# Optimization experiments

Hardware: AMD Instinct MI355X
Metric: run time of the kernel (lower is better)

Reference implementation:

```python
import jax, jax.numpy as jnp
import numpy as np

TEMP = 0.5  # init kwarg `tmp`
NUM_CLASSES = 100


def setup_inputs() -> dict:
    key = jax.random.key(0)
    k1, k2 = jax.random.split(key)
    embedding = jax.random.normal(k1, (8192, 256), dtype=jnp.float32)
    label = jax.random.randint(k2, (8192,), 0, NUM_CLASSES, dtype=jnp.int64)
    return {"embedding": embedding, "label": label}


def reference(embedding, label):
    # Row-normalize -> pairwise cosine similarity [N, N]
    normed = embedding / jnp.linalg.norm(embedding, axis=1, keepdims=True)
    sim = (normed @ normed.T) / TEMP  # already divided by temperature

    N = embedding.shape[0]
    eye = jnp.eye(N, dtype=bool)

    # Denominator: sum of exp(sim) over off-diagonal entries per row
    exp_sim = jnp.exp(sim)
    row_sum = jnp.sum(jnp.where(eye, 0.0, exp_sim), axis=1)  # [N]

    # log(exp(sim_ij) / row_sum_i) = sim_ij - log(row_sum_i)
    log_prob = sim - jnp.log(row_sum)[:, None]

    # Positive mask: same label, i != j
    pos_mask = (label[:, None] == label[None, :]) & ~eye
    n_i = jnp.sum(pos_mask, axis=1)  # positives per anchor

    inner = jnp.sum(jnp.where(pos_mask, log_prob, 0.0), axis=1)  # [N]
    per_anchor = jnp.where(n_i > 0, -inner / jnp.maximum(n_i, 1).astype(sim.dtype), 0.0)
    return jnp.sum(per_anchor)
```

## Files before the change

### kernel.cpp

```cpp
#include <hip/hip_runtime.h>
#include <hip/hip_bf16.h>
#include <stdint.h>

#define N    8192
#define D    256
#define NCLS 100

static constexpr float TEMP    = 0.5f;
static constexpr float SCALE_F = 1.69864360f;
static constexpr float LN2     = 0.69314718055994531f;

#define NSLOT 192

typedef float f32x4 __attribute__((ext_vector_type(4)));
typedef long  lx2  __attribute__((ext_vector_type(2)));

__device__ __forceinline__ unsigned short f2bf(float f) {
  union { float f; unsigned int u; } x; x.f = f;
  unsigned int r = x.u + 0x7fffu + ((x.u >> 16) & 1u);
  return (unsigned short)(r >> 16);
}
__device__ __forceinline__ float bf2f(unsigned short b) {
  union { unsigned int u; float f; } x; x.u = ((unsigned int)b) << 16;
  return x.f;
}


__global__ __launch_bounds__(256) void normalize_kernel(
    const float* __restrict__ emb, const long long* __restrict__ label,
    unsigned short* __restrict__ abf, unsigned char* __restrict__ a8,
    int* __restrict__ cnt, int* __restrict__ list) {
  const int row  = blockIdx.x * 4 + (threadIdx.x >> 6);
  const int lane = threadIdx.x & 63;
  const float4 v = ((const float4*)(emb + (size_t)row * D))[lane];
  float ss = v.x * v.x + v.y * v.y + v.z * v.z + v.w * v.w;
#pragma unroll
  for (int off = 1; off < 64; off <<= 1) ss += __shfl_xor(ss, off);
  const float s = rsqrtf(ss) * SCALE_F;
  const float x = v.x * s, y = v.y * s, z = v.z * s, wv = v.w * s;

  ushort4 o;
  o.x = f2bf(x); o.y = f2bf(y); o.z = f2bf(z); o.w = f2bf(wv);
  ((ushort4*)(abf + (size_t)row * D))[lane] = o;

  int p = __builtin_amdgcn_cvt_pk_fp8_f32(x, y, 0, false);
  p = __builtin_amdgcn_cvt_pk_fp8_f32(z, wv, p, true);
  *(int*)(a8 + (size_t)(row >> 4) * 4096 + (lane >> 4) * 1024 +
          ((lane >> 1) & 3) * 256 + (row & 15) * 16 + ((lane >> 3) & 1) * 8 +
          (lane & 1) * 4) = p;

  if (lane == 0) {
    const int c = (int)label[row];
    const int slot = atomicAdd(cnt + c, 1);
    list[c * 256 + slot] = row;
  }
}

__global__ __launch_bounds__(256, 2) void simexp_rowsum_kernel(
    const unsigned char* __restrict__ A, float* __restrict__ part) {
  const int tid  = threadIdx.x;
  const int w    = tid >> 6;
  const int lane = tid & 63;
  const int quad = lane >> 4;
  const int l15  = lane & 15;

  const int b = blockIdx.x;
  int y = 0, c = 0;
  while (c + ((65 - y) >> 1) <= b) { c += (65 - y) >> 1; ++y; }
  const int s = b - c;

  const int wm  = (w & 1) * 64;
  const int jn0 = (w >> 1) * 64;
  const int jh  = jn0 >> 6;
  const int wh  = wm >> 6;
  const bool diagstrip = (s == 0);

  const unsigned char* Ap = A + (size_t)(y * 8 + (w & 1) * 4) * 4096;
  const int lo = quad * 256 + l15 * 16;

  lx2 aF[4][4];
#pragma unroll
  for (int mt = 0; mt < 4; ++mt)
#pragma unroll
    for (int kq = 0; kq < 4; ++kq)
      aF[mt][kq] = *(const lx2*)(Ap + mt * 4096 + kq * 1024 + lo);

  float rowpart[4][4];
#pragma unroll
  for (int mt = 0; mt < 4; ++mt)
#pragma unroll
    for (int e = 0; e < 4; ++e) rowpart[mt][e] = 0.f;

#pragma unroll
  for (int t = 0; t < 2; ++t) {
    const int x = y + 2 * s + t;
    if (x >= 64) break;

    const unsigned char* Bp = A + (size_t)(x * 8 + (w >> 1) * 4) * 4096;
    lx2 bF[4][4];
#pragma unroll
    for (int nt = 0; nt < 4; ++nt)
#pragma unroll
      for (int kq = 0; kq < 4; ++kq)
        bF[nt][kq] = *(const lx2*)(Bp + nt * 4096 + kq * 1024 + lo);

    f32x4 acc[4][4];
#pragma unroll
    for (int mt = 0; mt < 4; ++mt)
#pragma unroll
      for (int nt = 0; nt < 4; ++nt)
        acc[mt][nt] = (f32x4){0.f, 0.f, 0.f, 0.f};

#pragma unroll
    for (int kq = 0; kq < 4; ++kq)
#pragma unroll
      for (int kkl = 0; kkl < 2; ++kkl)
#pragma unroll
        for (int mt = 0; mt < 4; ++mt)
#pragma unroll
          for (int nt = 0; nt < 4; ++nt)
            acc[mt][nt] = __builtin_amdgcn_mfma_f32_16x16x32_fp8_fp8(
                aF[mt][kq][kkl], bF[nt][kq][kkl], acc[mt][nt], 0, 0, 0);

    const bool dmask = diagstrip && (t == 0);
    float colpart[4] = {0.f, 0.f, 0.f, 0.f};
#pragma unroll
    for (int mt = 0; mt < 4; ++mt)
#pragma unroll
      for (int nt = 0; nt < 4; ++nt)
#pragma unroll
        for (int e = 0; e < 4; ++e) {
          float v = __builtin_amdgcn_exp2f(acc[mt][nt][e]);
          if (dmask) {
            const int iw = wm + mt * 16 + quad * 4 + e;
            const int jw = jn0 + nt * 16 + l15;
            v = (iw < jw) ? v : 0.f;
          }
          rowpart[mt][e] += v;
          colpart[nt] += v;
        }

    float* coldst = part + ((size_t)x * NSLOT + 64 + 2 * y + wh) * 128 + jn0;
#pragma unroll
    for (int nt = 0; nt < 4; ++nt) {
      float v = colpart[nt];
      v += __shfl_xor(v, 16);
      v += __shfl_xor(v, 32);
      if (quad == 0) coldst[nt * 16 + l15] = v;
    }
  }

  float* rowdst = part + ((size_t)y * NSLOT + 2 * s + jh) * 128 + wm;
#pragma unroll
  for (int mt = 0; mt < 4; ++mt)
#pragma unroll
    for (int e = 0; e < 4; ++e) {
      float v = rowpart[mt][e];
      v += __shfl_xor(v, 1);
      v += __shfl_xor(v, 2);
      v += __shfl_xor(v, 4);
      v += __shfl_xor(v, 8);
      if (l15 == 0) rowdst[mt * 16 + quad * 4 + e] = v;
    }
}

__global__ __launch_bounds__(256) void finalize_kernel(
    const unsigned short* __restrict__ abf, const float* __restrict__ part,
    const long long* __restrict__ label, const int* __restrict__ cnt,
    const int* __restrict__ list, float* __restrict__ out) {
  __shared__ float red[4];
  __shared__ int rows_l[256];
  const int tid  = threadIdx.x;
  const int w    = tid >> 6;
  const int lane = tid & 63;

  if (blockIdx.x < NCLS) {
    const int c = blockIdx.x;
    const int m = cnt[c];
    if (m <= 1) return;
    if (tid < m) rows_l[tid] = list[c * 256 + tid];
    __syncthreads();
    float acc = 0.f;
    for (int s = 0; s < m; ++s)
      acc += bf2f(abf[(size_t)rows_l[s] * D + tid]);
    float v = acc * acc;
#pragma unroll
    for (int off = 1; off < 64; off <<= 1) v += __shfl_xor(v, off);
    if (lane == 0) red[w] = v;
    __syncthreads();
    if (tid == 0) {
      const float ssq = red[0] + red[1] + red[2] + red[3];
      const float term = (ssq * LN2 - 2.0f * (float)m) / (float)(m - 1);
      atomicAdd(out, -term);
    }
  } else {
    const int i = (blockIdx.x - NCLS) * 256 + tid;
    const int band = i >> 7, r = i & 127;
    const float* ps = part + (size_t)band * NSLOT * 128 + r;
    const int rs_n = 2 * ((65 - band) >> 1);
    const int cs_n = 2 * band + 2;
    float rs = 0.f;
    for (int s2 = 0; s2 < rs_n; ++s2) rs += ps[(size_t)s2 * 128];
    for (int u = 0; u < cs_n; ++u) rs += ps[(size_t)(64 + u) * 128];
    const int c = (int)label[i];
    float v = 0.f;
    if (cnt[c] > 1)
      v = __builtin_amdgcn_logf(rs) * LN2;
#pragma unroll
    for (int off = 1; off < 64; off <<= 1) v += __shfl_xor(v, off);
    if (lane == 0) red[w] = v;
    __syncthreads();
    if (tid == 0)
      atomicAdd(out, red[0] + red[1] + red[2] + red[3]);
  }
}

extern "C" void kernel_launch(void* const* d_in, const int* in_sizes, int n_in,
                              void* d_out, int out_size, void* d_ws,
                              size_t ws_size, hipStream_t stream) {
  const float* emb = (const float*)d_in[0];
  const long long* label = (const long long*)d_in[1];
  float* out = (float*)d_out;

  char* ws = (char*)d_ws;
  unsigned short* abf = (unsigned short*)ws;
  unsigned char* a8 = (unsigned char*)(ws + (size_t)N * D * 2);
  float* part = (float*)(ws + (size_t)N * D * 3);
  int* cnt = (int*)(ws + (size_t)N * D * 3 + (size_t)64 * NSLOT * 128 * 4);
  int* list = cnt + 128;

  hipMemsetAsync(cnt, 0, 128 * 4, stream);
  hipMemsetAsync(out, 0, sizeof(float), stream);

  normalize_kernel<<<N / 4, 256, 0, stream>>>(emb, label, abf, a8, cnt, list);

  simexp_rowsum_kernel<<<1056, 256, 0, stream>>>(a8, part);

  finalize_kernel<<<NCLS + N / 256, 256, 0, stream>>>(abf, part, label, cnt,
                                                      list, out);
}
```

Baseline: 149.5 us.

## Prefetch second B tile before first epilogue and reindex partial-sum slots

```diff
diff --git a/kernel.cpp b/kernel.cpp
--- a/kernel.cpp
+++ b/kernel.cpp
@@ -10,7 +10,7 @@
 static constexpr float SCALE_F = 1.69864360f;
 static constexpr float LN2     = 0.69314718055994531f;
 
-#define NSLOT 192
+#define NSLOT 256
 
 typedef float f32x4 __attribute__((ext_vector_type(4)));
 typedef long  lx2  __attribute__((ext_vector_type(2)));
@@ -68,15 +68,17 @@
   int y = 0, c = 0;
   while (c + ((65 - y) >> 1) <= b) { c += (65 - y) >> 1; ++y; }
   const int s = b - c;
+  const int x0 = y + 2 * s;
+  const bool has1 = (x0 + 1 < 64);
+  const bool dmask = (s == 0);
 
   const int wm  = (w & 1) * 64;
   const int jn0 = (w >> 1) * 64;
   const int jh  = jn0 >> 6;
   const int wh  = wm >> 6;
-  const bool diagstrip = (s == 0);
+  const int lo  = quad * 256 + l15 * 16;
 
   const unsigned char* Ap = A + (size_t)(y * 8 + (w & 1) * 4) * 4096;
-  const int lo = quad * 256 + l15 * 16;
 
   lx2 aF[4][4];
 #pragma unroll
@@ -85,45 +87,47 @@
     for (int kq = 0; kq < 4; ++kq)
       aF[mt][kq] = *(const lx2*)(Ap + mt * 4096 + kq * 1024 + lo);
 
-  float rowpart[4][4];
+  const unsigned char* Bp0 = A + (size_t)(x0 * 8 + (w >> 1) * 4) * 4096;
+  lx2 bF[4][4];
+#pragma unroll
+  for (int nt = 0; nt < 4; ++nt)
+#pragma unroll
+    for (int kq = 0; kq < 4; ++kq)
+      bF[nt][kq] = *(const lx2*)(Bp0 + nt * 4096 + kq * 1024 + lo);
+
+  f32x4 acc[4][4];
 #pragma unroll
   for (int mt = 0; mt < 4; ++mt)
 #pragma unroll
-    for (int e = 0; e < 4; ++e) rowpart[mt][e] = 0.f;
-
-#pragma unroll
-  for (int t = 0; t < 2; ++t) {
-    const int x = y + 2 * s + t;
-    if (x >= 64) break;
-
-    const unsigned char* Bp = A + (size_t)(x * 8 + (w >> 1) * 4) * 4096;
-    lx2 bF[4][4];
+    for (int nt = 0; nt < 4; ++nt) acc[mt][nt] = (f32x4){0.f, 0.f, 0.f, 0.f};
+#pragma unroll
+  for (int kq = 0; kq < 4; ++kq)
+#pragma unroll
+    for (int kkl = 0; kkl < 2; ++kkl)
+#pragma unroll
+      for (int mt = 0; mt < 4; ++mt)
+#pragma unroll
+        for (int nt = 0; nt < 4; ++nt)
+          acc[mt][nt] = __builtin_amdgcn_mfma_f32_16x16x32_fp8_fp8(
+              aF[mt][kq][kkl], bF[nt][kq][kkl], acc[mt][nt], 0, 0, 0);
+
+  lx2 bG[4][4];
+  if (has1) {
+    const unsigned char* Bp1 = Bp0 + 8 * 4096;
 #pragma unroll
     for (int nt = 0; nt < 4; ++nt)
 #pragma unroll
       for (int kq = 0; kq < 4; ++kq)
-        bF[nt][kq] = *(const lx2*)(Bp + nt * 4096 + kq * 1024 + lo);
-
-    f32x4 acc[4][4];
-#pragma unroll
-    for (int mt = 0; mt < 4; ++mt)
-#pragma unroll
-      for (int nt = 0; nt < 4; ++nt)
-        acc[mt][nt] = (f32x4){0.f, 0.f, 0.f, 0.f};
-
-#pragma unroll
-    for (int kq = 0; kq < 4; ++kq)
-#pragma unroll
-      for (int kkl = 0; kkl < 2; ++kkl)
-#pragma unroll
-        for (int mt = 0; mt < 4; ++mt)
-#pragma unroll
-          for (int nt = 0; nt < 4; ++nt)
-            acc[mt][nt] = __builtin_amdgcn_mfma_f32_16x16x32_fp8_fp8(
-                aF[mt][kq][kkl], bF[nt][kq][kkl], acc[mt][nt], 0, 0, 0);
-
-    const bool dmask = diagstrip && (t == 0);
+        bG[nt][kq] = *(const lx2*)(Bp1 + nt * 4096 + kq * 1024 + lo);
+  }
+
+  {
+    float rowpart[4][4];
     float colpart[4] = {0.f, 0.f, 0.f, 0.f};
+#pragma unroll
+    for (int mt = 0; mt < 4; ++mt)
+#pragma unroll
+      for (int e = 0; e < 4; ++e) rowpart[mt][e] = 0.f;
 #pragma unroll
     for (int mt = 0; mt < 4; ++mt)
 #pragma unroll
@@ -139,8 +143,8 @@
           rowpart[mt][e] += v;
           colpart[nt] += v;
         }
-
-    float* coldst = part + ((size_t)x * NSLOT + 64 + 2 * y + wh) * 128 + jn0;
+    float* coldst =
+        part + ((size_t)x0 * NSLOT + 128 + 2 * y + wh) * 128 + jn0;
 #pragma unroll
     for (int nt = 0; nt < 4; ++nt) {
       float v = colpart[nt];
@@ -148,20 +152,77 @@
       v += __shfl_xor(v, 32);
       if (quad == 0) coldst[nt * 16 + l15] = v;
     }
-  }
-
-  float* rowdst = part + ((size_t)y * NSLOT + 2 * s + jh) * 128 + wm;
+    float* rowdst = part + ((size_t)y * NSLOT + 2 * x0 + jh) * 128 + wm;
+#pragma unroll
+    for (int mt = 0; mt < 4; ++mt)
+#pragma unroll
+      for (int e = 0; e < 4; ++e) {
+        float v = rowpart[mt][e];
+        v += __shfl_xor(v, 1);
+        v += __shfl_xor(v, 2);
+        v += __shfl_xor(v, 4);
+        v += __shfl_xor(v, 8);
+        if (l15 == 0) rowdst[mt * 16 + quad * 4 + e] = v;
+      }
+  }
+
+  if (!has1) return;
+
 #pragma unroll
   for (int mt = 0; mt < 4; ++mt)
 #pragma unroll
-    for (int e = 0; e < 4; ++e) {
-      float v = rowpart[mt][e];
-      v += __shfl_xor(v, 1);
-      v += __shfl_xor(v, 2);
-      v += __shfl_xor(v, 4);
-      v += __shfl_xor(v, 8);
-      if (l15 == 0) rowdst[mt * 16 + quad * 4 + e] = v;
+    for (int nt = 0; nt < 4; ++nt) acc[mt][nt] = (f32x4){0.f, 0.f, 0.f, 0.f};
+#pragma unroll
+  for (int kq = 0; kq < 4; ++kq)
+#pragma unroll
+    for (int kkl = 0; kkl < 2; ++kkl)
+#pragma unroll
+      for (int mt = 0; mt < 4; ++mt)
+#pragma unroll
+        for (int nt = 0; nt < 4; ++nt)
+          acc[mt][nt] = __builtin_amdgcn_mfma_f32_16x16x32_fp8_fp8(
+              aF[mt][kq][kkl], bG[nt][kq][kkl], acc[mt][nt], 0, 0, 0);
+
+  {
+    const int x1 = x0 + 1;
+    float rowpart[4][4];
+    float colpart[4] = {0.f, 0.f, 0.f, 0.f};
+#pragma unroll
+    for (int mt = 0; mt < 4; ++mt)
+#pragma unroll
+      for (int e = 0; e < 4; ++e) rowpart[mt][e] = 0.f;
+#pragma unroll
+    for (int mt = 0; mt < 4; ++mt)
+#pragma unroll
+      for (int nt = 0; nt < 4; ++nt)
+#pragma unroll
+        for (int e = 0; e < 4; ++e) {
+          float v = __builtin_amdgcn_exp2f(acc[mt][nt][e]);
+          rowpart[mt][e] += v;
+          colpart[nt] += v;
+        }
+    float* coldst =
+        part + ((size_t)x1 * NSLOT + 128 + 2 * y + wh) * 128 + jn0;
+#pragma unroll
+    for (int nt = 0; nt < 4; ++nt) {
+      float v = colpart[nt];
+      v += __shfl_xor(v, 16);
+      v += __shfl_xor(v, 32);
+      if (quad == 0) coldst[nt * 16 + l15] = v;
     }
+    float* rowdst = part + ((size_t)y * NSLOT + 2 * x1 + jh) * 128 + wm;
+#pragma unroll
+    for (int mt = 0; mt < 4; ++mt)
+#pragma unroll
+      for (int e = 0; e < 4; ++e) {
+        float v = rowpart[mt][e];
+        v += __shfl_xor(v, 1);
+        v += __shfl_xor(v, 2);
+        v += __shfl_xor(v, 4);
+        v += __shfl_xor(v, 8);
+        if (l15 == 0) rowdst[mt * 16 + quad * 4 + e] = v;
+      }
+  }
 }
 
 __global__ __launch_bounds__(256) void finalize_kernel(
@@ -197,11 +258,11 @@
     const int i = (blockIdx.x - NCLS) * 256 + tid;
     const int band = i >> 7, r = i & 127;
     const float* ps = part + (size_t)band * NSLOT * 128 + r;
-    const int rs_n = 2 * ((65 - band) >> 1);
-    const int cs_n = 2 * band + 2;
     float rs = 0.f;
-    for (int s2 = 0; s2 < rs_n; ++s2) rs += ps[(size_t)s2 * 128];
-    for (int u = 0; u < cs_n; ++u) rs += ps[(size_t)(64 + u) * 128];
+#pragma unroll 4
+    for (int s2 = 2 * band; s2 < 128; ++s2) rs += ps[(size_t)s2 * 128];
+#pragma unroll 4
+    for (int u = 128; u < 130 + 2 * band; ++u) rs += ps[(size_t)u * 128];
     const int c = (int)label[i];
     float v = 0.f;
     if (cnt[c] > 1)
```

Result: faster. 134.3 us (-10.2%).
